# Performance work log

Hardware: AMD Instinct MI355X
Metric: run time of the kernel (lower is better)

Reference implementation:

```python
import jax, jax.numpy as jnp
import numpy as np

B, N, DIM = 2, 2048, 1024
HEADS, DH, NUM_MEM = 8, 64, 4
EPS = 1e-5


def layer_norm(x, gamma):
    mu = x.mean(-1, keepdims=True)
    var = ((x - mu) ** 2).mean(-1, keepdims=True)
    return (x - mu) * jax.lax.rsqrt(var + EPS) * gamma


def setup_inputs() -> dict:
    key = jax.random.key(0)
    ks = jax.random.split(key, 7)
    x = jax.random.normal(ks[0], (B, N, DIM), jnp.float32)
    mask = jax.random.randint(ks[1], (B, N), 0, 2) > 0
    attn_bias = jax.random.normal(ks[2], (HEADS, N, N), jnp.float32) * 0.02
    gamma = jnp.ones((DIM,), jnp.float32)
    Wq = jax.random.normal(ks[3], (DIM, HEADS * DH), jnp.float32) * (DIM ** -0.5)
    Wkv = jax.random.normal(ks[4], (DIM, 2 * DH), jnp.float32) * (DIM ** -0.5)
    mem_kv = jax.random.normal(ks[5], (2, NUM_MEM, DH), jnp.float32)
    Wout = jax.random.normal(ks[6], (HEADS * DH, DIM), jnp.float32) * ((HEADS * DH) ** -0.5)
    return dict(x=x, attn_bias=attn_bias, gamma=gamma, Wq=Wq, Wkv=Wkv,
                mem_kv=mem_kv, Wout=Wout, mask=mask)


def reference(x, attn_bias, gamma, Wq, Wkv, mem_kv, Wout, mask):
    b, n, _ = x.shape
    # norm applied to query path only; kv comes from pre-norm x (self-attention)
    xn = layer_norm(x, gamma)
    q = (xn @ Wq).reshape(b, n, HEADS, DH).transpose(0, 2, 1, 3) * (DH ** -0.5)  # b h n d
    kv = x @ Wkv  # multi-query: single shared kv head
    k, v = kv[..., :DH], kv[..., DH:]
    mk = jnp.broadcast_to(mem_kv[0], (b, NUM_MEM, DH))
    mv = jnp.broadcast_to(mem_kv[1], (b, NUM_MEM, DH))
    k = jnp.concatenate([mk, k], axis=1)  # b (m+n) d
    v = jnp.concatenate([mv, v], axis=1)
    j = n + NUM_MEM
    bias = jnp.pad(attn_bias, ((0, 0), (0, 0), (NUM_MEM, 0)))  # zero bias on mem tokens
    maskp = jnp.pad(mask, ((0, 0), (NUM_MEM, 0)), constant_values=True)
    sim = jnp.einsum('bhid,bjd->bhij', q, k) + bias
    neg = -jnp.finfo(sim.dtype).max
    sim = jnp.where(maskp[:, None, None, :], sim, neg)
    causal = jnp.triu(jnp.ones((n, j), bool), k=NUM_MEM + 1)  # mem tokens always visible
    sim = jnp.where(causal, neg, sim)
    attn = jax.nn.softmax(sim, axis=-1)
    out = jnp.einsum('bhij,bjd->bhid', attn, v)
    out = out.transpose(0, 2, 1, 3).reshape(b, n, HEADS * DH)
    return out @ Wout
```

## Files before the change

### kernel.cpp

```cpp
#include <hip/hip_runtime.h>
#include <hip/hip_bf16.h>
#include <float.h>

#define B_ 2
#define N_ 2048
#define DIM_ 1024
#define HEADS_ 8
#define DH_ 64
#define NUM_MEM_ 4
#define ROWS_ (B_ * N_)
#define QCOLS_ (HEADS_ * DH_)
#define JTOT_ (N_ + NUM_MEM_)
#define JPAD_ 2176
#define CHUNKS_PER_BH_ 77

typedef __attribute__((ext_vector_type(8))) short short8v;
typedef __attribute__((ext_vector_type(4))) float f32x4;

static __device__ __forceinline__ ushort f2b(float f) {
    __hip_bfloat16 hb = __float2bfloat16(f);
    return *(ushort*)&hb;
}
static __device__ __forceinline__ uint pk2(float a, float b) {
    return ((uint)f2b(b) << 16) | (uint)f2b(a);
}
static __device__ __forceinline__ float b2f_lo(uint u) {
    union { uint x; float f; } c; c.x = u << 16; return c.f;
}
static __device__ __forceinline__ float b2f_hi(uint u) {
    union { uint x; float f; } c; c.x = u & 0xffff0000u; return c.f;
}

static __device__ __forceinline__ void wtrans_body(const float* __restrict__ W,
                                                   ushort* __restrict__ Wt,
                                                   int K, int N, int t) {
    int n = t % N;
    int k0 = (t / N) * 8;
    ushort u[8];
    #pragma unroll
    for (int j = 0; j < 8; ++j) u[j] = f2b(W[(size_t)(k0 + j) * N + n]);
    *(int4*)(Wt + (size_t)n * K + k0) = *(int4*)u;
}

__global__ __launch_bounds__(256) void ln_prep_kernel(const float* __restrict__ x,
                                                      const float* __restrict__ gamma,
                                                      const float* __restrict__ Wq,
                                                      const float* __restrict__ Wkv,
                                                      const float* __restrict__ Wout,
                                                      const float* __restrict__ mem_kv,
                                                      const int* __restrict__ mask,
                                                      ushort* __restrict__ xb,
                                                      ushort* __restrict__ xnb,
                                                      ushort* __restrict__ Wqt,
                                                      ushort* __restrict__ Wkvt,
                                                      ushort* __restrict__ Woutt,
                                                      ushort* __restrict__ Kb,
                                                      ushort* __restrict__ Vt,
                                                      ushort* __restrict__ amask) {
    int bid0 = blockIdx.x;
    if (bid0 < ROWS_) {
        int row = bid0;
        const float4 v = ((const float4*)(x + (size_t)row * DIM_))[threadIdx.x];
        float s  = v.x + v.y + v.z + v.w;
        float s2 = v.x * v.x + v.y * v.y + v.z * v.z + v.w * v.w;
        #pragma unroll
        for (int off = 32; off > 0; off >>= 1) {
            s  += __shfl_down(s, off);
            s2 += __shfl_down(s2, off);
        }
        __shared__ float ws1[4], ws2[4];
        int lane = threadIdx.x & 63, wid = threadIdx.x >> 6;
        if (lane == 0) { ws1[wid] = s; ws2[wid] = s2; }
        __syncthreads();
        float tot  = ws1[0] + ws1[1] + ws1[2] + ws1[3];
        float tot2 = ws2[0] + ws2[1] + ws2[2] + ws2[3];
        float mu  = tot * (1.0f / DIM_);
        float var = tot2 * (1.0f / DIM_) - mu * mu;
        float rs  = rsqrtf(var + 1e-5f);
        const float4 g = ((const float4*)gamma)[threadIdx.x];
        float vv[4] = {v.x, v.y, v.z, v.w};
        float gg[4] = {g.x, g.y, g.z, g.w};
        ushort xo[4], xno[4];
        #pragma unroll
        for (int j = 0; j < 4; ++j) {
            xo[j]  = f2b(vv[j]);
            xno[j] = f2b((vv[j] - mu) * rs * gg[j]);
        }
        *(int2*)(xb  + (size_t)row * DIM_ + threadIdx.x * 4) = *(int2*)xo;
        *(int2*)(xnb + (size_t)row * DIM_ + threadIdx.x * 4) = *(int2*)xno;
        return;
    }
    int bid = bid0 - ROWS_;
    int tid = threadIdx.x;
    if (bid < 256) {
        wtrans_body(Wq, Wqt, DIM_, QCOLS_, bid * 256 + tid);
    } else if (bid < 320) {
        wtrans_body(Wkv, Wkvt, DIM_, 2 * DH_, (bid - 256) * 256 + tid);
    } else if (bid < 576) {
        wtrans_body(Wout, Woutt, QCOLS_, DIM_, (bid - 320) * 256 + tid);
    } else if (bid < 640) {
        int t = (bid - 576) * 256 + tid;
        int d  = t & 63;
        int ji = (t >> 6) & 127;
        int b  = t >> 13;
        int j  = (ji < NUM_MEM_) ? ji : (2048 + ji);
        float kv_ = 0.f, vv = 0.f;
        if (ji < NUM_MEM_) {
            kv_ = mem_kv[ji * DH_ + d];
            vv  = mem_kv[NUM_MEM_ * DH_ + ji * DH_ + d];
        }
        Kb[((size_t)(b * JPAD_) + j) * DH_ + d] = f2b(kv_);
        Vt[((size_t)(b * DH_) + d) * JPAD_ + j] = f2b(vv);
    } else {
        int t = (bid - 640) * 256 + tid;
        if (t < B_ * JPAD_) {
            int b = t / JPAD_;
            int j = t % JPAD_;
            float v;
            if (j < NUM_MEM_) v = 0.f;
            else if (j < JTOT_) v = mask[b * N_ + (j - NUM_MEM_)] ? 0.f : -1e30f;
            else v = -1e30f;
            amask[(size_t)b * JPAD_ + j] = f2b(v);
        }
    }
}

template<int MODE>
static __device__ __forceinline__ void gemm64_body(ushort (*As)[40], ushort (*Bs)[40],
                                                   const ushort* __restrict__ A,
                                                   const ushort* __restrict__ Bt,
                                                   void* __restrict__ C,
                                                   void* __restrict__ C2,
                                                   int N, int K, int bx, int by) {
    int tid = threadIdx.x;
    int w = tid >> 6, l = tid & 63, lg = l >> 4, ll = l & 15;
    int r0 = by * 64, c0 = bx * 64;

    int arow = tid >> 2;
    int achk = (tid & 3) * 8;
    const ushort* Ap = A + (size_t)(r0 + arow) * K + achk;
    const ushort* Bp = Bt + (size_t)(c0 + arow) * K + achk;

    int4 a0 = *(const int4*)Ap;
    int4 b0 = *(const int4*)Bp;

    f32x4 acc[4] = {};

    int nk = K / 32;
    for (int ks = 0; ks < nk; ++ks) {
        __syncthreads();
        *(int4*)&As[arow][achk] = a0;
        *(int4*)&Bs[arow][achk] = b0;
        __syncthreads();
        int kn = (ks + 1 < nk) ? (ks + 1) * 32 : 0;
        a0 = *(const int4*)(Ap + kn);
        b0 = *(const int4*)(Bp + kn);
        short8v af, bf[4];
        af = *(const short8v*)&As[w * 16 + ll][lg * 8];
        #pragma unroll
        for (int ct = 0; ct < 4; ++ct)
            bf[ct] = *(const short8v*)&Bs[ct * 16 + ll][lg * 8];
        __builtin_amdgcn_s_setprio(1);
        #pragma unroll
        for (int ct = 0; ct < 4; ++ct)
            acc[ct] = __builtin_amdgcn_mfma_f32_16x16x32_bf16(af, bf[ct], acc[ct], 0, 0, 0);
        __builtin_amdgcn_s_setprio(0);
    }

    #pragma unroll
    for (int ct = 0; ct < 4; ++ct) {
        #pragma unroll
        for (int r = 0; r < 4; ++r) {
            int row = r0 + w * 16 + lg * 4 + r;
            int col = c0 + ct * 16 + ll;
            float val = acc[ct][r];
            if (MODE == 0) {
                ((ushort*)C)[(size_t)row * QCOLS_ + col] = f2b(val * 0.125f);
            } else {
                int b = row >> 11;
                int j = (row & 2047) + NUM_MEM_;
                if (col < DH_)
                    ((ushort*)C)[((size_t)(b * JPAD_) + j) * DH_ + col] = f2b(val);
                else
                    ((ushort*)C2)[((size_t)(b * DH_) + (col - DH_)) * JPAD_ + j] = f2b(val);
            }
        }
    }
}

__global__ __launch_bounds__(256) void gemm01_kernel(const ushort* __restrict__ xnb,
                                                     const ushort* __restrict__ Wqt,
                                                     ushort* __restrict__ qb,
                                                     const ushort* __restrict__ xb,
                                                     const ushort* __restrict__ Wkvt,
                                                     ushort* __restrict__ Kb,
                                                     ushort* __restrict__ Vt) {
    __shared__ ushort As[64][40];
    __shared__ ushort Bs[64][40];
    int bid = blockIdx.x;
    if (bid < 512) {
        gemm64_body<0>(As, Bs, xnb, Wqt, qb, nullptr, QCOLS_, DIM_, bid & 7, bid >> 3);
    } else {
        int r = bid - 512;
        gemm64_body<1>(As, Bs, xb, Wkvt, Kb, Vt, 2 * DH_, DIM_, r & 1, r >> 1);
    }
}

__global__ __launch_bounds__(256) void gemm_out_kernel(const ushort* __restrict__ A,
                                                       const ushort* __restrict__ Bt,
                                                       float* __restrict__ C,
                                                       int M, int N, int K) {
    __shared__ ushort As[128][40];
    __shared__ ushort Bs[64][40];
    int tid = threadIdx.x;
    int w = tid >> 6, l = tid & 63, lg = l >> 4, ll = l & 15;
    int r0 = blockIdx.y * 128, c0 = blockIdx.x * 64;

    int arow = tid >> 2;
    int achk = (tid & 3) * 8;
    const ushort* Ap  = A + (size_t)(r0 + arow) * K + achk;
    const ushort* Ap2 = Ap + (size_t)64 * K;
    const ushort* Bp  = Bt + (size_t)(c0 + arow) * K + achk;

    int4 a0 = *(const int4*)Ap;
    int4 a1 = *(const int4*)Ap2;
    int4 b0 = *(const int4*)Bp;

    f32x4 acc[2][4] = {};

    int nk = K / 32;
    for (int ks = 0; ks < nk; ++ks) {
        __syncthreads();
        *(int4*)&As[arow][achk]      = a0;
        *(int4*)&As[arow + 64][achk] = a1;
        *(int4*)&Bs[arow][achk]      = b0;
        __syncthreads();
        int kn = (ks + 1 < nk) ? (ks + 1) * 32 : 0;
        a0 = *(const int4*)(Ap + kn);
        a1 = *(const int4*)(Ap2 + kn);
        b0 = *(const int4*)(Bp + kn);
        short8v af[2], bf[4];
        af[0] = *(const short8v*)&As[w * 32 + ll][lg * 8];
        af[1] = *(const short8v*)&As[w * 32 + 16 + ll][lg * 8];
        #pragma unroll
        for (int ct = 0; ct < 4; ++ct)
            bf[ct] = *(const short8v*)&Bs[ct * 16 + ll][lg * 8];
        __builtin_amdgcn_s_setprio(1);
        #pragma unroll
        for (int rt = 0; rt < 2; ++rt)
            #pragma unroll
            for (int ct = 0; ct < 4; ++ct)
                acc[rt][ct] = __builtin_amdgcn_mfma_f32_16x16x32_bf16(af[rt], bf[ct], acc[rt][ct], 0, 0, 0);
        __builtin_amdgcn_s_setprio(0);
    }

    #pragma unroll
    for (int rt = 0; rt < 2; ++rt)
        #pragma unroll
        for (int ct = 0; ct < 4; ++ct)
            #pragma unroll
            for (int r = 0; r < 4; ++r) {
                int row = r0 + w * 32 + rt * 16 + lg * 4 + r;
                int col = c0 + ct * 16 + ll;
                C[(size_t)row * DIM_ + col] = acc[rt][ct][r];
            }
}

__global__ __launch_bounds__(256, 4) void fattn_split_kernel(const ushort* __restrict__ qb,
                                                             const ushort* __restrict__ Kb,
                                                             const ushort* __restrict__ Vt,
                                                             const float* __restrict__ bias,
                                                             const ushort* __restrict__ amask,
                                                             ushort* __restrict__ part_O,
                                                             float* __restrict__ part_ml,
                                                             ushort* __restrict__ attn_ob) {
    __shared__ ushort Ks[64][72];
    __shared__ ushort Vs[64][72];
    __shared__ ushort Bb[64][68];

    int cid = blockIdx.x;
    int bh  = cid / CHUNKS_PER_BH_;
    int rem = cid - bh * CHUNKS_PER_BH_;
    rem = CHUNKS_PER_BH_ - 1 - rem;
    int b = bh >> 3, h = bh & 7;
    int qt = 0, ci = 0;
    {
        int cum = 0;
        #pragma unroll 1
        for (int t = 0; t < 32; ++t) {
            int c = (t + 10) / 9;
            if (rem < cum + c) { qt = t; ci = rem - cum; break; }
            cum += c;
        }
    }
    int nt = qt + 2;
    int nc = (qt + 10) / 9;
    int t0 = ci * nt / nc;
    int t1 = (ci + 1) * nt / nc;
    int q0 = qt * 64;

    int tid = threadIdx.x;
    int w  = tid >> 6;
    int l  = tid & 63;
    int lg = l >> 4;
    int ll = l & 15;
    int i_row = q0 + w * 16 + ll;

    short8v aq0, aq1;
    {
        const ushort* qp = qb + ((size_t)(b * N_ + i_row)) * QCOLS_ + h * DH_;
        aq0 = *(const short8v*)(qp + lg * 8);
        aq1 = *(const short8v*)(qp + 32 + lg * 8);
    }

    int trow = tid >> 5;
    int tpc  = tid & 31;
    const float*  bias_rb = bias + ((size_t)h * N_ + q0 + trow) * N_;
    const ushort* am_row  = amask + (size_t)b * JPAD_;

    int sr = tid >> 3, sc = (tid & 7) * 8;
    const ushort* KbB = Kb + (size_t)b * JPAD_ * DH_;
    const ushort* VtB = Vt + (size_t)b * DH_ * JPAD_;

    int srcA = ((l & 16) << 1) + ll;
    int srcB = srcA + 16;
    bool hi = (l & 32) != 0;

    int jp0 = t0 * 64;
    int4 kr0 = *(const int4*)(KbB + (size_t)(jp0 + sr) * DH_ + sc);
    int4 kr1 = *(const int4*)(KbB + (size_t)(jp0 + sr + 32) * DH_ + sc);
    int4 vr0 = *(const int4*)(VtB + (size_t)sr * JPAD_ + jp0 + sc);
    int4 vr1 = *(const int4*)(VtB + (size_t)(sr + 32) * JPAD_ + jp0 + sc);

    uint bbc[8];
    {
        int j_e = jp0 + 2 * tpc;
        int sj  = j_e - NUM_MEM_;
        int sjc = sj < 0 ? 0 : (sj > N_ - 2 ? N_ - 2 : sj);
        uint am2 = *(const uint*)(am_row + j_e);
        float amf0 = b2f_lo(am2), amf1 = b2f_hi(am2);
        #pragma unroll
        for (int p = 0; p < 8; ++p) {
            float2 bv = *(const float2*)(bias_rb + (size_t)(8 * p) * N_ + sjc);
            int i_s = q0 + trow + 8 * p;
            float v0 = (j_e     < NUM_MEM_) ? 0.f : bv.x + amf0;
            float v1 = (j_e + 1 < NUM_MEM_) ? 0.f : bv.y + amf1;
            v0 = (j_e     <= i_s + NUM_MEM_) ? v0 : -1e30f;
            v1 = (j_e + 1 <= i_s + NUM_MEM_) ? v1 : -1e30f;
            bbc[p] = pk2(v0, v1);
        }
    }

    f32x4 oacc[4] = {};
    float mrow1 = -1e30f, lsum1 = 0.f;

    for (int jt = t0; jt < t1; ++jt) {
        __syncthreads();
        *(int4*)&Ks[sr][sc]      = kr0;
        *(int4*)&Ks[sr + 32][sc] = kr1;
        *(int4*)&Vs[sr][sc]      = vr0;
        *(int4*)&Vs[sr + 32][sc] = vr1;
        #pragma unroll
        for (int p = 0; p < 8; ++p)
            *(uint*)&Bb[trow + 8 * p][2 * tpc] = bbc[p];
        __syncthreads();

        int jn0 = (jt + 1 < t1 ? jt + 1 : jt) * 64;
        kr0 = *(const int4*)(KbB + (size_t)(jn0 + sr) * DH_ + sc);
        kr1 = *(const int4*)(KbB + (size_t)(jn0 + sr + 32) * DH_ + sc);
        vr0 = *(const int4*)(VtB + (size_t)sr * JPAD_ + jn0 + sc);
        vr1 = *(const int4*)(VtB + (size_t)(sr + 32) * JPAD_ + jn0 + sc);
        int j_e = jn0 + 2 * tpc;
        int sj  = j_e - NUM_MEM_;
        int sjc = sj < 0 ? 0 : (sj > N_ - 2 ? N_ - 2 : sj);
        uint am2n = *(const uint*)(am_row + j_e);
        float2 bvn[8];
        #pragma unroll
        for (int p = 0; p < 8; ++p)
            bvn[p] = *(const float2*)(bias_rb + (size_t)(8 * p) * N_ + sjc);

        float s[4][4];
        #pragma unroll
        for (int ct = 0; ct < 4; ++ct) {
            f32x4 acc = {};
            short8v bk0 = *(const short8v*)&Ks[ct * 16 + ll][lg * 8];
            short8v bk1 = *(const short8v*)&Ks[ct * 16 + ll][32 + lg * 8];
            __builtin_amdgcn_s_setprio(1);
            acc = __builtin_amdgcn_mfma_f32_16x16x32_bf16(bk0, aq0, acc, 0, 0, 0);
            acc = __builtin_amdgcn_mfma_f32_16x16x32_bf16(bk1, aq1, acc, 0, 0, 0);
            __builtin_amdgcn_s_setprio(0);
            uint2 ub = *(const uint2*)&Bb[w * 16 + ll][ct * 16 + lg * 4];
            s[ct][0] = acc[0] + b2f_lo(ub.x);
            s[ct][1] = acc[1] + b2f_hi(ub.x);
            s[ct][2] = acc[2] + b2f_lo(ub.y);
            s[ct][3] = acc[3] + b2f_hi(ub.y);
        }

        float m01 = fmaxf(fmaxf(s[0][0], s[0][1]), fmaxf(s[0][2], s[0][3]));
        float m23 = fmaxf(fmaxf(s[1][0], s[1][1]), fmaxf(s[1][2], s[1][3]));
        float m45 = fmaxf(fmaxf(s[2][0], s[2][1]), fmaxf(s[2][2], s[2][3]));
        float m67 = fmaxf(fmaxf(s[3][0], s[3][1]), fmaxf(s[3][2], s[3][3]));
        float m = fmaxf(fmaxf(m01, m23), fmaxf(m45, m67));
        m = fmaxf(m, __shfl_xor(m, 16));
        m = fmaxf(m, __shfl_xor(m, 32));
        float mn = fmaxf(mrow1, m);
        float scl = __expf(mrow1 - mn);
        mrow1 = mn;

        float ps = 0.f;
        #pragma unroll
        for (int ct = 0; ct < 4; ++ct)
            #pragma unroll
            for (int r = 0; r < 4; ++r) {
                float p = __expf(s[ct][r] - mn);
                s[ct][r] = p;
                ps += p;
            }
        ps += __shfl_xor(ps, 16);
        ps += __shfl_xor(ps, 32);
        lsum1 = lsum1 * scl + ps;

        uint pux[4], puy[4];
        #pragma unroll
        for (int ct = 0; ct < 4; ++ct) {
            pux[ct] = pk2(s[ct][0], s[ct][1]);
            puy[ct] = pk2(s[ct][2], s[ct][3]);
        }
        #pragma unroll
        for (int dt = 0; dt < 4; ++dt)
            #pragma unroll
            for (int r = 0; r < 4; ++r) oacc[dt][r] *= scl;

        #pragma unroll
        for (int c = 0; c < 2; ++c) {
            int cl = 2 * c, ch = 2 * c + 1;
            uint xA_l = (uint)__shfl((int)pux[cl], srcA);
            uint xA_h = (uint)__shfl((int)pux[ch], srcA);
            uint yA_l = (uint)__shfl((int)puy[cl], srcA);
            uint yA_h = (uint)__shfl((int)puy[ch], srcA);
            uint xB_l = (uint)__shfl((int)pux[cl], srcB);
            uint xB_h = (uint)__shfl((int)pux[ch], srcB);
            uint yB_l = (uint)__shfl((int)puy[cl], srcB);
            uint yB_h = (uint)__shfl((int)puy[ch], srcB);
            uint uu[4];
            uu[0] = hi ? xA_h : xA_l;
            uu[1] = hi ? yA_h : yA_l;
            uu[2] = hi ? xB_h : xB_l;
            uu[3] = hi ? yB_h : yB_l;
            short8v ptf = *(const short8v*)uu;
            __builtin_amdgcn_s_setprio(1);
            #pragma unroll
            for (int dt = 0; dt < 4; ++dt) {
                short8v bv = *(const short8v*)&Vs[dt * 16 + ll][c * 32 + lg * 8];
                oacc[dt] = __builtin_amdgcn_mfma_f32_16x16x32_bf16(bv, ptf, oacc[dt], 0, 0, 0);
            }
            __builtin_amdgcn_s_setprio(0);
        }

        {
            float amf0 = b2f_lo(am2n), amf1 = b2f_hi(am2n);
            #pragma unroll
            for (int p = 0; p < 8; ++p) {
                int i_s = q0 + trow + 8 * p;
                float v0 = (j_e     < NUM_MEM_) ? 0.f : bvn[p].x + amf0;
                float v1 = (j_e + 1 < NUM_MEM_) ? 0.f : bvn[p].y + amf1;
                v0 = (j_e     <= i_s + NUM_MEM_) ? v0 : -1e30f;
                v1 = (j_e + 1 <= i_s + NUM_MEM_) ? v1 : -1e30f;
                bbc[p] = pk2(v0, v1);
            }
        }
    }

    if (nc == 1) {
        float inv = 1.f / lsum1;
        ushort* dst = attn_ob + ((size_t)(b * N_ + i_row)) * QCOLS_ + h * DH_;
        #pragma unroll
        for (int dt = 0; dt < 4; ++dt) {
            uint2 pu;
            pu.x = pk2(oacc[dt][0] * inv, oacc[dt][1] * inv);
            pu.y = pk2(oacc[dt][2] * inv, oacc[dt][3] * inv);
            *(uint2*)(dst + dt * 16 + lg * 4) = pu;
        }
    } else {
        int bh_s = b * 8 + h;
        int slot = (bh_s * 32 + qt) * 4 + ci;
        ushort* po = part_O + (size_t)slot * 4096;
        #pragma unroll
        for (int dt = 0; dt < 4; ++dt) {
            uint2 pu;
            pu.x = pk2(oacc[dt][0], oacc[dt][1]);
            pu.y = pk2(oacc[dt][2], oacc[dt][3]);
            *(uint2*)&po[(w * 16 + ll) * 64 + dt * 16 + lg * 4] = pu;
        }
        if (lg == 0) {
            part_ml[(size_t)slot * 128 + (w * 16 + ll) * 2]     = mrow1;
            part_ml[(size_t)slot * 128 + (w * 16 + ll) * 2 + 1] = lsum1;
        }
    }
}

__global__ __launch_bounds__(256) void merge_kernel(const ushort* __restrict__ part_O,
                                                    const float* __restrict__ part_ml,
                                                    ushort* __restrict__ attn_ob) {
    int bid = blockIdx.x;
    int qt = bid & 31;
    int nc = (qt + 10) / 9;
    if (nc < 2) return;
    int bh = bid >> 5;
    int b = bh >> 3, h = bh & 7;
    int tid = threadIdx.x;
    int row = tid >> 2;
    int dseg = (tid & 3) * 16;
    int slot0 = bid * 4;

    float M = -1e30f;
    #pragma unroll
    for (int c = 0; c < 4; ++c) {
        if (c >= nc) break;
        M = fmaxf(M, part_ml[(size_t)(slot0 + c) * 128 + row * 2]);
    }
    float den = 0.f;
    float num[16] = {};
    #pragma unroll
    for (int c = 0; c < 4; ++c) {
        if (c >= nc) break;
        float m_c = part_ml[(size_t)(slot0 + c) * 128 + row * 2];
        float l_c = part_ml[(size_t)(slot0 + c) * 128 + row * 2 + 1];
        float wgt = __expf(m_c - M);
        den += wgt * l_c;
        const uint4* src = (const uint4*)(part_O + (size_t)(slot0 + c) * 4096 + row * 64 + dseg);
        uint4 v0 = src[0];
        uint4 v1 = src[1];
        uint uu[8] = { v0.x, v0.y, v0.z, v0.w, v1.x, v1.y, v1.z, v1.w };
        #pragma unroll
        for (int e = 0; e < 8; ++e) {
            num[e * 2 + 0] += wgt * b2f_lo(uu[e]);
            num[e * 2 + 1] += wgt * b2f_hi(uu[e]);
        }
    }
    float inv = 1.f / den;
    ushort o[16];
    #pragma unroll
    for (int e = 0; e < 16; ++e) o[e] = f2b(num[e] * inv);
    int i = qt * 64 + row;
    ushort* dst = attn_ob + ((size_t)(b * N_ + i)) * QCOLS_ + h * DH_ + dseg;
    *(int4*)dst = *(int4*)o;
    *(int4*)(dst + 8) = *(int4*)(o + 8);
}

extern "C" void kernel_launch(void* const* d_in, const int* in_sizes, int n_in,
                              void* d_out, int out_size, void* d_ws, size_t ws_size,
                              hipStream_t stream) {
    const float* x         = (const float*)d_in[0];
    const float* attn_bias = (const float*)d_in[1];
    const float* gamma     = (const float*)d_in[2];
    const float* Wq        = (const float*)d_in[3];
    const float* Wkv       = (const float*)d_in[4];
    const float* mem_kv    = (const float*)d_in[5];
    const float* Wout      = (const float*)d_in[6];
    const int*   mask      = (const int*)d_in[7];
    float* out = (float*)d_out;

    char* wsb = (char*)d_ws;
    ushort* xb      = (ushort*)wsb;
    ushort* xnb     = (ushort*)(wsb + (8u  << 20));
    ushort* qb      = (ushort*)(wsb + (16u << 20));
    ushort* attn_ob = (ushort*)(wsb + (20u << 20));
    ushort* Kb      = (ushort*)(wsb + (24u << 20));
    ushort* Vt      = (ushort*)(wsb + (25u << 20));
    ushort* Wqt     = (ushort*)(wsb + (26u << 20));
    ushort* Wkvt    = (ushort*)(wsb + (27u << 20));
    ushort* Woutt   = (ushort*)(wsb + (28u << 20));
    ushort* amask   = (ushort*)(wsb + (29u << 20));
    ushort* part_O  = (ushort*)(wsb + (32u << 20));
    float*  part_ml = (float*)(wsb + (64u << 20));

    ln_prep_kernel<<<ROWS_ + 657, 256, 0, stream>>>(x, gamma, Wq, Wkv, Wout, mem_kv, mask,
                                                    xb, xnb, Wqt, Wkvt, Woutt, Kb, Vt, amask);
    gemm01_kernel<<<640, 256, 0, stream>>>(xnb, Wqt, qb, xb, Wkvt, Kb, Vt);
    fattn_split_kernel<<<16 * CHUNKS_PER_BH_, 256, 0, stream>>>(qb, Kb, Vt, attn_bias, amask,
                                                                part_O, part_ml, attn_ob);
    merge_kernel<<<512, 256, 0, stream>>>(part_O, part_ml, attn_ob);
    gemm_out_kernel<<<dim3(DIM_ / 64, ROWS_ / 128), 256, 0, stream>>>(attn_ob, Woutt, out, ROWS_, DIM_, QCOLS_);
}
```

Before: 94.92 us.

## Fuse split-KV merge into attention kernel via last-block atomic counter

Removes the separate merge kernel launch. Each attention split block increments a per-strip atomic counter after writing its partial output, and the last block to finish merges all partials for that strip in place. The counters are zeroed by an extra block in the prep kernel. This saves a launch and the gap between kernels, at the cost of extra fences, atomics and a tail of merge work inside the attention kernel.

```diff
diff --git a/kernel.cpp b/kernel.cpp
--- a/kernel.cpp
+++ b/kernel.cpp
@@ -56,7 +56,8 @@
                                                       ushort* __restrict__ Woutt,
                                                       ushort* __restrict__ Kb,
                                                       ushort* __restrict__ Vt,
-                                                      ushort* __restrict__ amask) {
+                                                      ushort* __restrict__ amask,
+                                                      uint* __restrict__ chunk_cnt) {
     int bid0 = blockIdx.x;
     if (bid0 < ROWS_) {
         int row = bid0;
@@ -111,7 +112,7 @@
         }
         Kb[((size_t)(b * JPAD_) + j) * DH_ + d] = f2b(kv_);
         Vt[((size_t)(b * DH_) + d) * JPAD_ + j] = f2b(vv);
-    } else {
+    } else if (bid < 657) {
         int t = (bid - 640) * 256 + tid;
         if (t < B_ * JPAD_) {
             int b = t / JPAD_;
@@ -122,6 +123,9 @@
             else v = -1e30f;
             amask[(size_t)b * JPAD_ + j] = f2b(v);
         }
+    } else {
+        chunk_cnt[tid]       = 0u;
+        chunk_cnt[tid + 256] = 0u;
     }
 }
 
@@ -266,6 +270,54 @@
             }
 }
 
+static __device__ __forceinline__ void merge_strip(int strip,
+                                                   const ushort* __restrict__ part_O,
+                                                   const float* __restrict__ part_ml,
+                                                   ushort* __restrict__ attn_ob) {
+    int qt = strip & 31;
+    int nc = (qt + 10) / 9;
+    int bh = strip >> 5;
+    int b = bh >> 3, h = bh & 7;
+    int tid = threadIdx.x;
+    int row = tid >> 2;
+    int dseg = (tid & 3) * 16;
+    int slot0 = strip * 4;
+
+    float M = -1e30f;
+    #pragma unroll
+    for (int c = 0; c < 4; ++c) {
+        if (c >= nc) break;
+        M = fmaxf(M, part_ml[(size_t)(slot0 + c) * 128 + row * 2]);
+    }
+    float den = 0.f;
+    float num[16] = {};
+    #pragma unroll
+    for (int c = 0; c < 4; ++c) {
+        if (c >= nc) break;
+        float m_c = part_ml[(size_t)(slot0 + c) * 128 + row * 2];
+        float l_c = part_ml[(size_t)(slot0 + c) * 128 + row * 2 + 1];
+        float wgt = __expf(m_c - M);
+        den += wgt * l_c;
+        const uint4* src = (const uint4*)(part_O + (size_t)(slot0 + c) * 4096 + row * 64 + dseg);
+        uint4 v0 = src[0];
+        uint4 v1 = src[1];
+        uint uu[8] = { v0.x, v0.y, v0.z, v0.w, v1.x, v1.y, v1.z, v1.w };
+        #pragma unroll
+        for (int e = 0; e < 8; ++e) {
+            num[e * 2 + 0] += wgt * b2f_lo(uu[e]);
+            num[e * 2 + 1] += wgt * b2f_hi(uu[e]);
+        }
+    }
+    float inv = 1.f / den;
+    ushort o[16];
+    #pragma unroll
+    for (int e = 0; e < 16; ++e) o[e] = f2b(num[e] * inv);
+    int i = qt * 64 + row;
+    ushort* dst = attn_ob + ((size_t)(b * N_ + i)) * QCOLS_ + h * DH_ + dseg;
+    *(int4*)dst = *(int4*)o;
+    *(int4*)(dst + 8) = *(int4*)(o + 8);
+}
+
 __global__ __launch_bounds__(256, 4) void fattn_split_kernel(const ushort* __restrict__ qb,
                                                              const ushort* __restrict__ Kb,
                                                              const ushort* __restrict__ Vt,
@@ -273,10 +325,12 @@
                                                              const ushort* __restrict__ amask,
                                                              ushort* __restrict__ part_O,
                                                              float* __restrict__ part_ml,
-                                                             ushort* __restrict__ attn_ob) {
+                                                             ushort* __restrict__ attn_ob,
+                                                             uint* __restrict__ chunk_cnt) {
     __shared__ ushort Ks[64][72];
     __shared__ ushort Vs[64][72];
     __shared__ ushort Bb[64][68];
+    __shared__ int last_flag;
 
     int cid = blockIdx.x;
     int bh  = cid / CHUNKS_PER_BH_;
@@ -482,8 +536,8 @@
             *(uint2*)(dst + dt * 16 + lg * 4) = pu;
         }
     } else {
-        int bh_s = b * 8 + h;
-        int slot = (bh_s * 32 + qt) * 4 + ci;
+        int strip = bh * 32 + qt;
+        int slot = strip * 4 + ci;
         ushort* po = part_O + (size_t)slot * 4096;
         #pragma unroll
         for (int dt = 0; dt < 4; ++dt) {
@@ -496,56 +550,19 @@
             part_ml[(size_t)slot * 128 + (w * 16 + ll) * 2]     = mrow1;
             part_ml[(size_t)slot * 128 + (w * 16 + ll) * 2 + 1] = lsum1;
         }
-    }
-}
-
-__global__ __launch_bounds__(256) void merge_kernel(const ushort* __restrict__ part_O,
-                                                    const float* __restrict__ part_ml,
-                                                    ushort* __restrict__ attn_ob) {
-    int bid = blockIdx.x;
-    int qt = bid & 31;
-    int nc = (qt + 10) / 9;
-    if (nc < 2) return;
-    int bh = bid >> 5;
-    int b = bh >> 3, h = bh & 7;
-    int tid = threadIdx.x;
-    int row = tid >> 2;
-    int dseg = (tid & 3) * 16;
-    int slot0 = bid * 4;
-
-    float M = -1e30f;
-    #pragma unroll
-    for (int c = 0; c < 4; ++c) {
-        if (c >= nc) break;
-        M = fmaxf(M, part_ml[(size_t)(slot0 + c) * 128 + row * 2]);
-    }
-    float den = 0.f;
-    float num[16] = {};
-    #pragma unroll
-    for (int c = 0; c < 4; ++c) {
-        if (c >= nc) break;
-        float m_c = part_ml[(size_t)(slot0 + c) * 128 + row * 2];
-        float l_c = part_ml[(size_t)(slot0 + c) * 128 + row * 2 + 1];
-        float wgt = __expf(m_c - M);
-        den += wgt * l_c;
-        const uint4* src = (const uint4*)(part_O + (size_t)(slot0 + c) * 4096 + row * 64 + dseg);
-        uint4 v0 = src[0];
-        uint4 v1 = src[1];
-        uint uu[8] = { v0.x, v0.y, v0.z, v0.w, v1.x, v1.y, v1.z, v1.w };
-        #pragma unroll
-        for (int e = 0; e < 8; ++e) {
-            num[e * 2 + 0] += wgt * b2f_lo(uu[e]);
-            num[e * 2 + 1] += wgt * b2f_hi(uu[e]);
-        }
-    }
-    float inv = 1.f / den;
-    ushort o[16];
-    #pragma unroll
-    for (int e = 0; e < 16; ++e) o[e] = f2b(num[e] * inv);
-    int i = qt * 64 + row;
-    ushort* dst = attn_ob + ((size_t)(b * N_ + i)) * QCOLS_ + h * DH_ + dseg;
-    *(int4*)dst = *(int4*)o;
-    *(int4*)(dst + 8) = *(int4*)(o + 8);
+
+        __syncthreads();
+        if (tid == 0) {
+            __threadfence();
+            uint prev = atomicAdd(&chunk_cnt[strip], 1u);
+            last_flag = (prev == (uint)(nc - 1));
+        }
+        __syncthreads();
+        if (last_flag) {
+            __threadfence();
+            merge_strip(strip, part_O, part_ml, attn_ob);
+        }
+    }
 }
 
 extern "C" void kernel_launch(void* const* d_in, const int* in_sizes, int n_in,
@@ -562,24 +579,24 @@
     float* out = (float*)d_out;
 
     char* wsb = (char*)d_ws;
-    ushort* xb      = (ushort*)wsb;
-    ushort* xnb     = (ushort*)(wsb + (8u  << 20));
-    ushort* qb      = (ushort*)(wsb + (16u << 20));
-    ushort* attn_ob = (ushort*)(wsb + (20u << 20));
-    ushort* Kb      = (ushort*)(wsb + (24u << 20));
-    ushort* Vt      = (ushort*)(wsb + (25u << 20));
-    ushort* Wqt     = (ushort*)(wsb + (26u << 20));
-    ushort* Wkvt    = (ushort*)(wsb + (27u << 20));
-    ushort* Woutt   = (ushort*)(wsb + (28u << 20));
-    ushort* amask   = (ushort*)(wsb + (29u << 20));
-    ushort* part_O  = (ushort*)(wsb + (32u << 20));
-    float*  part_ml = (float*)(wsb + (64u << 20));
-
-    ln_prep_kernel<<<ROWS_ + 657, 256, 0, stream>>>(x, gamma, Wq, Wkv, Wout, mem_kv, mask,
-                                                    xb, xnb, Wqt, Wkvt, Woutt, Kb, Vt, amask);
+    ushort* xb        = (ushort*)wsb;
+    ushort* xnb       = (ushort*)(wsb + (8u  << 20));
+    ushort* qb        = (ushort*)(wsb + (16u << 20));
+    ushort* attn_ob   = (ushort*)(wsb + (20u << 20));
+    ushort* Kb        = (ushort*)(wsb + (24u << 20));
+    ushort* Vt        = (ushort*)(wsb + (25u << 20));
+    ushort* Wqt       = (ushort*)(wsb + (26u << 20));
+    ushort* Wkvt      = (ushort*)(wsb + (27u << 20));
+    ushort* Woutt     = (ushort*)(wsb + (28u << 20));
+    ushort* amask     = (ushort*)(wsb + (29u << 20));
+    uint*   chunk_cnt = (uint*)(wsb + (30u << 20));
+    ushort* part_O    = (ushort*)(wsb + (32u << 20));
+    float*  part_ml   = (float*)(wsb + (64u << 20));
+
+    ln_prep_kernel<<<ROWS_ + 658, 256, 0, stream>>>(x, gamma, Wq, Wkv, Wout, mem_kv, mask,
+                                                    xb, xnb, Wqt, Wkvt, Woutt, Kb, Vt, amask, chunk_cnt);
     gemm01_kernel<<<640, 256, 0, stream>>>(xnb, Wqt, qb, xb, Wkvt, Kb, Vt);
     fattn_split_kernel<<<16 * CHUNKS_PER_BH_, 256, 0, stream>>>(qb, Kb, Vt, attn_bias, amask,
-                                                                part_O, part_ml, attn_ob);
-    merge_kernel<<<512, 256, 0, stream>>>(part_O, part_ml, attn_ob);
+                                                                part_O, part_ml, attn_ob, chunk_cnt);
     gemm_out_kernel<<<dim3(DIM_ / 64, ROWS_ / 128), 256, 0, stream>>>(attn_ob, Woutt, out, ROWS_, DIM_, QCOLS_);
 }
```

Result: slower. 254.1 us (+167.7%).
